# Kernel optimization log

Measured on AMD Instinct MI355X. Metric: run time of the kernel, lower is better.

The kernel has to match this reference:

```python
import jax, jax.numpy as jnp
import numpy as np

C = 512
GROUPS = 8
EPS = 1e-5


def setup_inputs() -> dict:
    key = jax.random.key(0)
    ks = jax.random.split(key, 11)
    B, H, W = 8, 64, 64
    x = jax.random.normal(ks[0], (B, C, H, W), dtype=jnp.float32)
    s = 1.0 / np.sqrt(C)
    return {
        "x": x,
        "gn_w": jnp.ones((C,), jnp.float32),
        "gn_b": jnp.zeros((C,), jnp.float32),
        "wq": jax.random.normal(ks[1], (C, C), jnp.float32) * s,
        "bq": jnp.zeros((C,), jnp.float32),
        "wk": jax.random.normal(ks[2], (C, C), jnp.float32) * s,
        "bk": jnp.zeros((C,), jnp.float32),
        "wv": jax.random.normal(ks[3], (C, C), jnp.float32) * s,
        "bv": jnp.zeros((C,), jnp.float32),
        "wo": jax.random.normal(ks[4], (C, C), jnp.float32) * s,
        "bo": jnp.zeros((C,), jnp.float32),
    }


def _group_norm(x, w, b):
    # x: [B, C, H, W], 8 groups over channel dim
    B, Ch, H, W = x.shape
    xg = x.reshape(B, GROUPS, Ch // GROUPS, H, W)
    mu = jnp.mean(xg, axis=(2, 3, 4), keepdims=True)
    var = jnp.var(xg, axis=(2, 3, 4), keepdims=True)
    xn = ((xg - mu) * jax.lax.rsqrt(var + EPS)).reshape(B, Ch, H, W)
    return xn * w[None, :, None, None] + b[None, :, None, None]


def reference(x, gn_w, gn_b, wq, bq, wk, bk, wv, bv, wo, bo):
    B, Ch, H, W = x.shape
    h = _group_norm(x, gn_w, gn_b)
    # [B, N, C] tokens, N = H*W
    h = h.reshape(B, Ch, H * W).transpose(0, 2, 1)
    q = jnp.einsum('bnc,dc->bnd', h, wq) + bq
    k = jnp.einsum('bnc,dc->bnd', h, wk) + bk
    v = jnp.einsum('bnc,dc->bnd', h, wv) + bv
    scores = jnp.einsum('bnd,bmd->bnm', q, k) / jnp.sqrt(jnp.float32(Ch))
    attn = jax.nn.softmax(scores, axis=-1)
    out = jnp.einsum('bnm,bmd->bnd', attn, v)
    out = jnp.einsum('bnd,ed->bne', out, wo) + bo
    out = out.transpose(0, 2, 1).reshape(B, Ch, H, W)
    return x + out
```

## Files before the change

### kernel.cpp

```cpp
#include <hip/hip_runtime.h>
#include <hip/hip_bf16.h>
#include <stdint.h>

typedef __hip_bfloat16 bf16;
typedef unsigned short u16;
typedef unsigned int u32;
using short8  = __attribute__((ext_vector_type(8))) short;
using short4v = __attribute__((ext_vector_type(4))) short;
using floatx4 = __attribute__((ext_vector_type(4))) float;
using uintx4  = __attribute__((ext_vector_type(4))) u32;

#define SCALE_L2E 0.06375872f

__device__ __forceinline__ float b2f(u16 u) {
  union { u32 i; float f; } v; v.i = ((u32)u) << 16; return v.f;
}
__device__ __forceinline__ u16 f2b(float f) {
  union { float f; u32 i; } v; v.f = f;
  u32 r = v.i + 0x7fffu + ((v.i >> 16) & 1u);
  return (u16)(r >> 16);
}

__device__ __forceinline__ void gl2lds16(const void* g, void* l) {
  __builtin_amdgcn_global_load_lds(
      (const __attribute__((address_space(1))) void*)g,
      (__attribute__((address_space(3))) void*)l,
      16, 0, 0);
}

__global__ __launch_bounds__(256)
void cvt_weights(const float* __restrict__ w0, const float* __restrict__ w1,
                 const float* __restrict__ w2, const float* __restrict__ w3,
                 u16* __restrict__ o0, u16* __restrict__ o1,
                 u16* __restrict__ o2, u16* __restrict__ o3)
{
  const float* w = blockIdx.y == 0 ? w0 : blockIdx.y == 1 ? w1 : blockIdx.y == 2 ? w2 : w3;
  u16* o = blockIdx.y == 0 ? o0 : blockIdx.y == 1 ? o1 : blockIdx.y == 2 ? o2 : o3;
  const int i = (blockIdx.x * 256 + threadIdx.x) * 4;
  floatx4 v = *(const floatx4*)(w + i);
  short4v p;
#pragma unroll
  for (int j = 0; j < 4; j++) p[j] = (short)f2b(v[j]);
  *(short4v*)(o + i) = p;
}

__global__ __launch_bounds__(256)
void gn_stats(const float* __restrict__ x, float* __restrict__ gmean, float* __restrict__ grstd)
{
  const int g = blockIdx.x, b = blockIdx.y;
  const float* base = x + ((long)(b * 512 + g * 64)) * 4096;
  const int t = threadIdx.x;
  float s = 0.f, ss = 0.f;
  for (int i = 0; i < 256; i++) {
    floatx4 v = *(const floatx4*)(base + i * 1024 + t * 4);
#pragma unroll
    for (int j = 0; j < 4; j++) { s += v[j]; ss += v[j] * v[j]; }
  }
  for (int off = 1; off < 64; off <<= 1) {
    s  += __shfl_xor(s, off, 64);
    ss += __shfl_xor(ss, off, 64);
  }
  __shared__ float as_[4], ass_[4];
  if ((t & 63) == 0) { as_[t >> 6] = s; ass_[t >> 6] = ss; }
  __syncthreads();
  if (t == 0) {
    float S1 = as_[0] + as_[1] + as_[2] + as_[3];
    float S2 = ass_[0] + ass_[1] + ass_[2] + ass_[3];
    const float inv = 1.0f / 262144.0f;
    float mu = S1 * inv;
    float var = S2 * inv - mu * mu;
    gmean[b * 8 + g] = mu;
    grstd[b * 8 + g] = rsqrtf(var + 1e-5f);
  }
}

__global__ __launch_bounds__(256)
void gn_apply(const float* __restrict__ x, const float* __restrict__ gw, const float* __restrict__ gb,
              const float* __restrict__ gmean, const float* __restrict__ grstd,
              bf16* __restrict__ h)
{
  const int b = blockIdx.z;
  const int c0 = blockIdx.y * 64;
  const int p0 = blockIdx.x * 64;
  const int t = threadIdx.x;
  const int c = c0 + (t & 63);
  const int g = c >> 6;
  const float mu = gmean[b * 8 + g], rs = grstd[b * 8 + g];
  const float wv = gw[c];
  const float bv = gb[c];
  const float a = rs * wv;
  const float bb = bv - mu * rs * wv;
  const float* xp = x + ((long)(b * 512 + c)) * 4096;
  u16* hp = (u16*)h + ((long)b * 4096) * 512 + c;
  const int pbase = p0 + (t >> 6);
#pragma unroll
  for (int i = 0; i < 16; i++) {
    int p = pbase + i * 4;
    float xv = xp[p];
    hp[(long)p * 512] = f2b(xv * a + bb);
  }
}

__global__ __launch_bounds__(256)
void pv_reduce(const bf16* __restrict__ part, const float* __restrict__ rl,
               bf16* __restrict__ o, long sOz, int RS)
{
  const int z = blockIdx.x;
  const long base = (long)blockIdx.y * 1024 + threadIdx.x * 4;
  const long slab = (long)RS * 512;
  const u16* p = (const u16*)part + (long)z * 4 * slab + base;
  floatx4 s = (floatx4)0.f;
#pragma unroll
  for (int sp = 0; sp < 4; sp++) {
    short4v v = *(const short4v*)(p + sp * slab);
#pragma unroll
    for (int j = 0; j < 4; j++) s[j] += b2f((u16)v[j]);
  }
  const float r = 1.0f / rl[z * RS + (int)(base >> 9)];
  short4v ov;
#pragma unroll
  for (int j = 0; j < 4; j++) ov[j] = (short)f2b(s[j] * r);
  *(short4v*)((u16*)o + (long)z * sOz + base) = ov;
}

constexpr int BM = 128, BN = 128, BK = 32;

template<int MODE>
__global__ __launch_bounds__(256)
void gemm_bt(const bf16* __restrict__ Ag, long sA,
             const bf16* __restrict__ Bg, long sB,
             const float* __restrict__ bias,
             const float* __restrict__ bias2,
             const float* __restrict__ bias3,
             const float* __restrict__ resid, long sR,
             bf16* __restrict__ Og, long sO, long sO2,
             float* __restrict__ rl,
             int M, int N, int K)
{
  __shared__ u16 As[2][BM * BK];
  __shared__ u16 Bs[2][BN * BK];
  const int t = threadIdx.x;
  const int bz = blockIdx.x;
  const int bm = blockIdx.y;
  int bn = blockIdx.z, sp = 0, kbeg = 0, kend = K;
  if (MODE == 3) { sp = bn >> 2; bn &= 3; kbeg = sp * 1024; kend = kbeg + 1024; }

  const u16* A = (const u16*)Ag + (long)bz * sA;
  const u16* B = (const u16*)Bg + (long)bz * sB;

  const int lane = t & 63, w = t >> 6;

  const int rs_ = w * 16 + (lane >> 2);
  const int seg = ((lane & 3) ^ ((rs_ >> 1) & 3)) * 8;
  const long aOff  = (long)(bm * BM + rs_) * K + seg;
  const long bOff  = (long)(bn * BN + rs_) * K + seg;
  const long aOff2 = aOff + 64L * K;
  const long bOff2 = bOff + 64L * K;
  const int wofs = w * 1024;

  const int wm = (w >> 1) * 64, wn = (w & 1) * 64;
  const int lc = lane & 15, quad = lane >> 4;

  int aoffs[4], boffs[4];
#pragma unroll
  for (int i = 0; i < 4; i++) {
    const int Ra = wm + i * 16 + lc;
    const int Rb = wn + i * 16 + lc;
    aoffs[i] = Ra * 64 + ((quad ^ ((Ra >> 1) & 3)) * 16);
    boffs[i] = Rb * 64 + ((quad ^ ((Rb >> 1) & 3)) * 16);
  }

  floatx4 acc[4][4];
#pragma unroll
  for (int i = 0; i < 4; i++)
#pragma unroll
    for (int j = 0; j < 4; j++) acc[i][j] = (floatx4)0.f;

  auto stage = [&](int buf, int kk) {
    char* aw = (char*)&As[buf][0] + wofs;
    char* bw = (char*)&Bs[buf][0] + wofs;
    gl2lds16(A + aOff  + kk, aw);
    gl2lds16(A + aOff2 + kk, aw + 4096);
    gl2lds16(B + bOff  + kk, bw);
    gl2lds16(B + bOff2 + kk, bw + 4096);
  };

  stage(0, kbeg);
  int cur = 0;
  for (int kk = kbeg; kk < kend; kk += BK) {
    __syncthreads();
    if (kk + BK < kend) stage(cur ^ 1, kk + BK);
    const char* Ac = (const char*)&As[cur][0];
    const char* Bc = (const char*)&Bs[cur][0];
    short8 af[4], bfr[4];
#pragma unroll
    for (int i = 0; i < 4; i++) af[i]  = *(const short8*)(Ac + aoffs[i]);
#pragma unroll
    for (int j = 0; j < 4; j++) bfr[j] = *(const short8*)(Bc + boffs[j]);
#pragma unroll
    for (int i = 0; i < 4; i++)
#pragma unroll
      for (int j = 0; j < 4; j++)
        acc[i][j] = __builtin_amdgcn_mfma_f32_16x16x32_bf16(af[i], bfr[j], acc[i][j], 0, 0, 0);
    cur ^= 1;
  }

#pragma unroll
  for (int i = 0; i < 4; i++) {
    const int gm0 = bm * BM + wm + i * 16 + quad * 4;
    if (MODE == 2) {
      u16* Ou = (u16*)(Og + (long)bz * sO);
      float rsum[4] = {0.f, 0.f, 0.f, 0.f};
#pragma unroll
      for (int j = 0; j < 4; j++) {
        const int gn = bn * BN + wn + j * 16 + lc;
        floatx4 a = acc[i][j];
#pragma unroll
        for (int rg = 0; rg < 4; rg++) {
          float p = exp2f(a[rg] * SCALE_L2E);
          rsum[rg] += p;
          Ou[(long)(gm0 + rg) * N + gn] = f2b(p);
        }
      }
#pragma unroll
      for (int rg = 0; rg < 4; rg++) {
        float s = rsum[rg];
        s += __shfl_xor(s, 1, 64);
        s += __shfl_xor(s, 2, 64);
        s += __shfl_xor(s, 4, 64);
        s += __shfl_xor(s, 8, 64);
        if (lc == 0) atomicAdd(&rl[(long)bz * M + gm0 + rg], s);
      }
    } else {
#pragma unroll
      for (int j = 0; j < 4; j++) {
        const int gn = bn * BN + wn + j * 16 + lc;
        floatx4 a = acc[i][j];
        if (MODE == 3) {
          u16* Ou = (u16*)Og + (long)(bz * 4 + sp) * sO;
#pragma unroll
          for (int rg = 0; rg < 4; rg++)
            Ou[(long)(gm0 + rg) * N + gn] = f2b(a[rg]);
        } else if (MODE == 4) {
          float* Of = (float*)Og + (long)bz * sO;
          const float bv = bias[gn];
          const float* Rz = resid + (long)bz * sR;
          const floatx4 rv = *(const floatx4*)&Rz[(long)gn * M + gm0];
          floatx4 p;
#pragma unroll
          for (int rg = 0; rg < 4; rg++) p[rg] = a[rg] + bv + rv[rg];
          *(floatx4*)&Of[(long)gn * M + gm0] = p;
        } else if (MODE == 5) {
          const int nt = gn >> 9;
          const int col = gn & 511;
          const float bvv = (nt == 0 ? bias : nt == 1 ? bias2 : bias3)[col];
          u16* Ou = (u16*)Og + (long)nt * sO2 + (long)bz * sO;
          if (nt < 2) {
#pragma unroll
            for (int rg = 0; rg < 4; rg++)
              Ou[(long)(gm0 + rg) * 512 + col] = f2b(a[rg] + bvv);
          } else {
            short4v p;
#pragma unroll
            for (int rg = 0; rg < 4; rg++) p[rg] = (short)f2b(a[rg] + bvv);
            *(short4v*)&Ou[(long)col * M + gm0] = p;
          }
        }
      }
    }
  }
}

extern "C" void kernel_launch(void* const* d_in, const int* in_sizes, int n_in,
                              void* d_out, int out_size, void* d_ws, size_t ws_size,
                              hipStream_t stream)
{
  const float* x  = (const float*)d_in[0];
  const float* gw = (const float*)d_in[1];
  const float* gb = (const float*)d_in[2];
  const float* wq = (const float*)d_in[3];
  const float* bq = (const float*)d_in[4];
  const float* wk = (const float*)d_in[5];
  const float* bk = (const float*)d_in[6];
  const float* wv = (const float*)d_in[7];
  const float* bv = (const float*)d_in[8];
  const float* wo = (const float*)d_in[9];
  const float* bo = (const float*)d_in[10];

  const long PB = (long)4096 * 512;

  auto need = [&](long nb, long rs) -> size_t {
    return (size_t)(4 * 262144 * 2
                  + nb * PB * 2 * 4
                  + nb * rs * 4096 * 2
                  + nb * 4 * rs * 512 * 2
                  + nb * 4096 * 4
                  + 8192);
  };
  const long cand_nB[4] = {8, 4, 2, 1};
  const long cand_RS[2] = {1024, 512};
  long nB = 1, RS = 512;
  bool found = false;
  for (int i = 0; i < 4 && !found; i++)
    for (int j = 0; j < 2 && !found; j++)
      if (need(cand_nB[i], cand_RS[j]) <= ws_size) { nB = cand_nB[i]; RS = cand_RS[j]; found = true; }

  char* ws = (char*)d_ws;
  u16*   wqb  = (u16*)ws;
  u16*   wkb  = wqb + 262144;
  u16*   wvb  = wkb + 262144;
  u16*   wob  = wvb + 262144;
  bf16*  h    = (bf16*)(wob + 262144);
  bf16*  q    = h  + nB * PB;
  bf16*  k    = q  + nB * PB;
  bf16*  vT   = k  + nB * PB;
  bf16*  o    = h;
  bf16*  S    = vT + nB * PB;
  bf16*  part = S + nB * RS * 4096;
  float* rl   = (float*)(part + nB * 4 * RS * 512);
  float* gm   = rl + nB * 4096;
  float* gr   = gm + 64;

  const long sS = RS * 4096;

  cvt_weights<<<dim3(256, 4), 256, 0, stream>>>(wq, wk, wv, wo, wqb, wkb, wvb, wob);
  gn_stats<<<dim3(8, 8), 256, 0, stream>>>(x, gm, gr);

  for (long b0 = 0; b0 < 8; b0 += nB) {
    const int gs = (int)nB;

    gn_apply<<<dim3(64, 8, gs), 256, 0, stream>>>(x + b0 * PB, gw, gb, gm + b0 * 8, gr + b0 * 8, h);
    hipMemsetAsync(rl, 0, (size_t)gs * 4096 * sizeof(float), stream);

    gemm_bt<5><<<dim3(gs, 32, 12), 256, 0, stream>>>(
        h, PB, (bf16*)wqb, 0, bq, bk, bv, nullptr, 0,
        q, PB, nB * PB, nullptr, 4096, 1536, 512);

    for (long r0 = 0; r0 < 4096; r0 += RS) {
      float* rli = rl + (r0 / RS) * (long)gs * RS;
      gemm_bt<2><<<dim3(gs, (int)(RS / 128), 32), 256, 0, stream>>>(
          q + r0 * 512, PB, k, PB, nullptr, nullptr, nullptr, nullptr, 0,
          S, sS, 0, rli, (int)RS, 4096, 512);
      gemm_bt<3><<<dim3(gs, (int)(RS / 128), 16), 256, 0, stream>>>(
          S, sS, vT, PB, nullptr, nullptr, nullptr, nullptr, 0,
          part, (long)RS * 512, 0, nullptr, (int)RS, 512, 4096);
      pv_reduce<<<dim3(gs, (int)(RS / 2)), 256, 0, stream>>>(
          part, rli, o + r0 * 512, PB, (int)RS);
    }

    gemm_bt<4><<<dim3(gs, 32, 4), 256, 0, stream>>>(
        o, PB, (bf16*)wob, 0, bo, nullptr, nullptr,
        x + b0 * PB, PB, (bf16*)((float*)d_out + b0 * PB), PB, 0, nullptr, 4096, 512, 512);
  }
}
```

Measured before the change: 792.7 us.

## Fuse QK, softmax and PV into one flash-style attention kernel

Replaces the separate score GEMM, split-K PV GEMM and reduction kernels with a single fused kernel. Each block computes a 128-query tile, streams 128-key chunks, exponentiates scores into LDS and accumulates the full 512-wide output in registers, normalizing by row sums at the end. This removes the global round trip of the score matrix, the partial buffers, the memset and the atomics. In exchange it has heavy register and LDS use, a grid of only one block per query tile, and reloads Q for every key chunk.

```diff
diff --git a/kernel.cpp b/kernel.cpp
--- a/kernel.cpp
+++ b/kernel.cpp
@@ -101,28 +101,6 @@
   }
 }
 
-__global__ __launch_bounds__(256)
-void pv_reduce(const bf16* __restrict__ part, const float* __restrict__ rl,
-               bf16* __restrict__ o, long sOz, int RS)
-{
-  const int z = blockIdx.x;
-  const long base = (long)blockIdx.y * 1024 + threadIdx.x * 4;
-  const long slab = (long)RS * 512;
-  const u16* p = (const u16*)part + (long)z * 4 * slab + base;
-  floatx4 s = (floatx4)0.f;
-#pragma unroll
-  for (int sp = 0; sp < 4; sp++) {
-    short4v v = *(const short4v*)(p + sp * slab);
-#pragma unroll
-    for (int j = 0; j < 4; j++) s[j] += b2f((u16)v[j]);
-  }
-  const float r = 1.0f / rl[z * RS + (int)(base >> 9)];
-  short4v ov;
-#pragma unroll
-  for (int j = 0; j < 4; j++) ov[j] = (short)f2b(s[j] * r);
-  *(short4v*)((u16*)o + (long)z * sOz + base) = ov;
-}
-
 constexpr int BM = 128, BN = 128, BK = 32;
 
 template<int MODE>
@@ -134,7 +112,6 @@
              const float* __restrict__ bias3,
              const float* __restrict__ resid, long sR,
              bf16* __restrict__ Og, long sO, long sO2,
-             float* __restrict__ rl,
              int M, int N, int K)
 {
   __shared__ u16 As[2][BM * BK];
@@ -142,8 +119,7 @@
   const int t = threadIdx.x;
   const int bz = blockIdx.x;
   const int bm = blockIdx.y;
-  int bn = blockIdx.z, sp = 0, kbeg = 0, kend = K;
-  if (MODE == 3) { sp = bn >> 2; bn &= 3; kbeg = sp * 1024; kend = kbeg + 1024; }
+  const int bn = blockIdx.z;
 
   const u16* A = (const u16*)Ag + (long)bz * sA;
   const u16* B = (const u16*)Bg + (long)bz * sB;
@@ -185,11 +161,11 @@
     gl2lds16(B + bOff2 + kk, bw + 4096);
   };
 
-  stage(0, kbeg);
+  stage(0, 0);
   int cur = 0;
-  for (int kk = kbeg; kk < kend; kk += BK) {
+  for (int kk = 0; kk < K; kk += BK) {
     __syncthreads();
-    if (kk + BK < kend) stage(cur ^ 1, kk + BK);
+    if (kk + BK < K) stage(cur ^ 1, kk + BK);
     const char* Ac = (const char*)&As[cur][0];
     const char* Bc = (const char*)&Bs[cur][0];
     short8 af[4], bfr[4];
@@ -208,67 +184,216 @@
 #pragma unroll
   for (int i = 0; i < 4; i++) {
     const int gm0 = bm * BM + wm + i * 16 + quad * 4;
-    if (MODE == 2) {
-      u16* Ou = (u16*)(Og + (long)bz * sO);
-      float rsum[4] = {0.f, 0.f, 0.f, 0.f};
-#pragma unroll
-      for (int j = 0; j < 4; j++) {
-        const int gn = bn * BN + wn + j * 16 + lc;
-        floatx4 a = acc[i][j];
-#pragma unroll
-        for (int rg = 0; rg < 4; rg++) {
-          float p = exp2f(a[rg] * SCALE_L2E);
-          rsum[rg] += p;
-          Ou[(long)(gm0 + rg) * N + gn] = f2b(p);
-        }
-      }
-#pragma unroll
-      for (int rg = 0; rg < 4; rg++) {
-        float s = rsum[rg];
-        s += __shfl_xor(s, 1, 64);
-        s += __shfl_xor(s, 2, 64);
-        s += __shfl_xor(s, 4, 64);
-        s += __shfl_xor(s, 8, 64);
-        if (lc == 0) atomicAdd(&rl[(long)bz * M + gm0 + rg], s);
-      }
-    } else {
-#pragma unroll
-      for (int j = 0; j < 4; j++) {
-        const int gn = bn * BN + wn + j * 16 + lc;
-        floatx4 a = acc[i][j];
-        if (MODE == 3) {
-          u16* Ou = (u16*)Og + (long)(bz * 4 + sp) * sO;
+#pragma unroll
+    for (int j = 0; j < 4; j++) {
+      const int gn = bn * BN + wn + j * 16 + lc;
+      floatx4 a = acc[i][j];
+      if (MODE == 4) {
+        float* Of = (float*)Og + (long)bz * sO;
+        const float bv = bias[gn];
+        const float* Rz = resid + (long)bz * sR;
+        const floatx4 rv = *(const floatx4*)&Rz[(long)gn * M + gm0];
+        floatx4 p;
+#pragma unroll
+        for (int rg = 0; rg < 4; rg++) p[rg] = a[rg] + bv + rv[rg];
+        *(floatx4*)&Of[(long)gn * M + gm0] = p;
+      } else {
+        const int nt = gn >> 9;
+        const int col = gn & 511;
+        const float bvv = (nt == 0 ? bias : nt == 1 ? bias2 : bias3)[col];
+        u16* Ou = (u16*)Og + (long)nt * sO2 + (long)bz * sO;
+        if (nt < 2) {
 #pragma unroll
           for (int rg = 0; rg < 4; rg++)
-            Ou[(long)(gm0 + rg) * N + gn] = f2b(a[rg]);
-        } else if (MODE == 4) {
-          float* Of = (float*)Og + (long)bz * sO;
-          const float bv = bias[gn];
-          const float* Rz = resid + (long)bz * sR;
-          const floatx4 rv = *(const floatx4*)&Rz[(long)gn * M + gm0];
-          floatx4 p;
-#pragma unroll
-          for (int rg = 0; rg < 4; rg++) p[rg] = a[rg] + bv + rv[rg];
-          *(floatx4*)&Of[(long)gn * M + gm0] = p;
-        } else if (MODE == 5) {
-          const int nt = gn >> 9;
-          const int col = gn & 511;
-          const float bvv = (nt == 0 ? bias : nt == 1 ? bias2 : bias3)[col];
-          u16* Ou = (u16*)Og + (long)nt * sO2 + (long)bz * sO;
-          if (nt < 2) {
-#pragma unroll
-            for (int rg = 0; rg < 4; rg++)
-              Ou[(long)(gm0 + rg) * 512 + col] = f2b(a[rg] + bvv);
-          } else {
-            short4v p;
-#pragma unroll
-            for (int rg = 0; rg < 4; rg++) p[rg] = (short)f2b(a[rg] + bvv);
-            *(short4v*)&Ou[(long)col * M + gm0] = p;
-          }
+            Ou[(long)(gm0 + rg) * 512 + col] = f2b(a[rg] + bvv);
+        } else {
+          short4v p;
+#pragma unroll
+          for (int rg = 0; rg < 4; rg++) p[rg] = (short)f2b(a[rg] + bvv);
+          *(short4v*)&Ou[(long)col * M + gm0] = p;
         }
       }
     }
   }
+}
+
+#define COMPUTE_SLAB(S, BUF)                                                \
+  {                                                                         \
+    _Pragma("unroll")                                                       \
+    for (int ks = 0; ks < 4; ks++) {                                        \
+      short8 vf[2], pf[4];                                                  \
+      _Pragma("unroll")                                                     \
+      for (int mf = 0; mf < 2; mf++) {                                      \
+        const int r = wr * 32 + mf * 16 + lc;                               \
+        vf[mf] = *(const short8*)((const char*)&vt_s[BUF][0] +              \
+                   r * 256 + (((ks * 4 + quad) ^ (r & 7)) * 16));           \
+      }                                                                     \
+      _Pragma("unroll")                                                     \
+      for (int nf = 0; nf < 4; nf++) {                                      \
+        const int r = wc * 64 + nf * 16 + lc;                               \
+        pf[nf] = *(const short8*)((const char*)p_s +                        \
+                   r * 256 + (((ks * 4 + quad) ^ (r & 7)) * 16));           \
+      }                                                                     \
+      _Pragma("unroll")                                                     \
+      for (int mf = 0; mf < 2; mf++)                                        \
+        _Pragma("unroll")                                                   \
+        for (int nf = 0; nf < 4; nf++)                                      \
+          acc_o[S][mf][nf] = __builtin_amdgcn_mfma_f32_16x16x32_bf16(       \
+              vf[mf], pf[nf], acc_o[S][mf][nf], 0, 0, 0);                   \
+    }                                                                       \
+  }
+
+__global__ __launch_bounds__(512, 2)
+void fused_attn(const bf16* __restrict__ qg, const bf16* __restrict__ kg,
+                const bf16* __restrict__ vtg, bf16* __restrict__ og)
+{
+  __shared__ u16 qk_s[2][2][128 * 32];
+  __shared__ u16 vt_s[2][128 * 128];
+  __shared__ u16 p_s[128 * 128];
+  __shared__ float rsum_s[4][128];
+
+  const int t = threadIdx.x;
+  const int lane = t & 63, w = t >> 6;
+  const int lc = lane & 15, quad = lane >> 4;
+  const int wr = w >> 1, wc = w & 1;
+  const int z = blockIdx.x, qt = blockIdx.y;
+  const long zoff = (long)z * (4096L * 512);
+  const u16* q_z  = (const u16*)qg + zoff;
+  const u16* k_z  = (const u16*)kg + zoff;
+  const u16* vt_z = (const u16*)vtg + zoff;
+  u16* o_z = (u16*)og + zoff;
+
+  const int srow = t >> 2;
+  const int sseg = ((t & 3) ^ ((srow >> 1) & 3)) * 8;
+  const u16* qsrc  = q_z + (long)(qt * 128 + srow) * 512 + sseg;
+  const u16* ksrcC = k_z + (long)srow * 512 + sseg;
+  const int vrow = t >> 4;
+  const int vseg = ((t & 15) ^ (vrow & 7)) * 8;
+  const u16* vsrcC = vt_z + (long)vrow * 4096 + vseg;
+
+  const int ldsbase = w * 1024;
+
+  int koff[2], qoff[4];
+#pragma unroll
+  for (int mf = 0; mf < 2; mf++) {
+    const int r = wr * 32 + mf * 16 + lc;
+    koff[mf] = r * 64 + ((quad ^ ((r >> 1) & 3)) * 16);
+  }
+#pragma unroll
+  for (int nf = 0; nf < 4; nf++) {
+    const int r = wc * 64 + nf * 16 + lc;
+    qoff[nf] = r * 64 + ((quad ^ ((r >> 1) & 3)) * 16);
+  }
+
+  auto stage_qk = [&](int buf, int ds) {
+    char* base = (char*)&qk_s[buf][0][0] + ldsbase;
+    gl2lds16(qsrc  + ds * 32, base);
+    gl2lds16(ksrcC + ds * 32, base + 8192);
+  };
+  auto stage_vt = [&](int buf, int slab) {
+    char* base = (char*)&vt_s[buf][0] + ldsbase;
+    const u16* vs = vsrcC + (long)slab * (128L * 4096);
+#pragma unroll
+    for (int i = 0; i < 4; i++)
+      gl2lds16(vs + (long)i * (32L * 4096), base + i * 8192);
+  };
+
+  floatx4 acc_o[4][2][4];
+#pragma unroll
+  for (int s = 0; s < 4; s++)
+#pragma unroll
+    for (int mf = 0; mf < 2; mf++)
+#pragma unroll
+      for (int nf = 0; nf < 4; nf++) acc_o[s][mf][nf] = (floatx4)0.f;
+  float rsum[4] = {0.f, 0.f, 0.f, 0.f};
+
+  for (int ck = 0; ck < 32; ++ck) {
+    floatx4 acc_s[2][4];
+#pragma unroll
+    for (int mf = 0; mf < 2; mf++)
+#pragma unroll
+      for (int nf = 0; nf < 4; nf++) acc_s[mf][nf] = (floatx4)0.f;
+
+    stage_qk(0, 0);
+#pragma unroll 2
+    for (int ds = 0; ds < 16; ++ds) {
+      __syncthreads();
+      if (ds < 15) stage_qk((ds + 1) & 1, ds + 1);
+      else         stage_vt(0, 0);
+      const int b = ds & 1;
+      const char* Kc = (const char*)&qk_s[b][1][0];
+      const char* Qc = (const char*)&qk_s[b][0][0];
+      short8 kf[2], qf[4];
+#pragma unroll
+      for (int mf = 0; mf < 2; mf++) kf[mf] = *(const short8*)(Kc + koff[mf]);
+#pragma unroll
+      for (int nf = 0; nf < 4; nf++) qf[nf] = *(const short8*)(Qc + qoff[nf]);
+#pragma unroll
+      for (int mf = 0; mf < 2; mf++)
+#pragma unroll
+        for (int nf = 0; nf < 4; nf++)
+          acc_s[mf][nf] = __builtin_amdgcn_mfma_f32_16x16x32_bf16(kf[mf], qf[nf], acc_s[mf][nf], 0, 0, 0);
+    }
+
+#pragma unroll
+    for (int mf = 0; mf < 2; mf++)
+#pragma unroll
+      for (int nf = 0; nf < 4; nf++) {
+        floatx4 a = acc_s[mf][nf];
+        float p0 = exp2f(a[0] * SCALE_L2E);
+        float p1 = exp2f(a[1] * SCALE_L2E);
+        float p2 = exp2f(a[2] * SCALE_L2E);
+        float p3 = exp2f(a[3] * SCALE_L2E);
+        rsum[nf] += (p0 + p1) + (p2 + p3);
+        short4v pk;
+        pk[0] = (short)f2b(p0); pk[1] = (short)f2b(p1);
+        pk[2] = (short)f2b(p2); pk[3] = (short)f2b(p3);
+        const int key0 = wr * 32 + mf * 16 + quad * 4;
+        const int qq = wc * 64 + nf * 16 + lc;
+        *(short4v*)((char*)p_s + qq * 256 + ((key0 * 2) ^ ((qq & 7) << 4))) = pk;
+      }
+
+    __syncthreads();
+    stage_vt(1, 1);
+    COMPUTE_SLAB(0, 0)
+    __syncthreads();
+    stage_vt(0, 2);
+    COMPUTE_SLAB(1, 1)
+    __syncthreads();
+    stage_vt(1, 3);
+    COMPUTE_SLAB(2, 0)
+    __syncthreads();
+    COMPUTE_SLAB(3, 1)
+
+    ksrcC += 128 * 512;
+    vsrcC += 128;
+  }
+
+#pragma unroll
+  for (int nf = 0; nf < 4; nf++) {
+    float s = rsum[nf];
+    s += __shfl_xor(s, 16, 64);
+    s += __shfl_xor(s, 32, 64);
+    if (lane < 16) rsum_s[wr][wc * 64 + nf * 16 + lane] = s;
+  }
+  __syncthreads();
+
+#pragma unroll
+  for (int s = 0; s < 4; s++)
+#pragma unroll
+    for (int mf = 0; mf < 2; mf++)
+#pragma unroll
+      for (int nf = 0; nf < 4; nf++) {
+        const int qq = wc * 64 + nf * 16 + lc;
+        const float tot = (rsum_s[0][qq] + rsum_s[1][qq]) + (rsum_s[2][qq] + rsum_s[3][qq]);
+        const float r = 1.0f / tot;
+        floatx4 a = acc_o[s][mf][nf];
+        short4v ov;
+#pragma unroll
+        for (int rg = 0; rg < 4; rg++) ov[rg] = (short)f2b(a[rg] * r);
+        const int d0 = s * 128 + wr * 32 + mf * 16 + quad * 4;
+        *(short4v*)&o_z[(long)(qt * 128 + qq) * 512 + d0] = ov;
+      }
 }
 
 extern "C" void kernel_launch(void* const* d_in, const int* in_sizes, int n_in,
@@ -289,21 +414,13 @@
 
   const long PB = (long)4096 * 512;
 
-  auto need = [&](long nb, long rs) -> size_t {
-    return (size_t)(4 * 262144 * 2
-                  + nb * PB * 2 * 4
-                  + nb * rs * 4096 * 2
-                  + nb * 4 * rs * 512 * 2
-                  + nb * 4096 * 4
-                  + 8192);
+  auto need = [&](long nb) -> size_t {
+    return (size_t)(4 * 262144 * 2 + nb * PB * 2 * 4 + 8192);
   };
+  long nB = 1;
   const long cand_nB[4] = {8, 4, 2, 1};
-  const long cand_RS[2] = {1024, 512};
-  long nB = 1, RS = 512;
-  bool found = false;
-  for (int i = 0; i < 4 && !found; i++)
-    for (int j = 0; j < 2 && !found; j++)
-      if (need(cand_nB[i], cand_RS[j]) <= ws_size) { nB = cand_nB[i]; RS = cand_RS[j]; found = true; }
+  for (int i = 0; i < 4; i++)
+    if (need(cand_nB[i]) <= ws_size) { nB = cand_nB[i]; break; }
 
   char* ws = (char*)d_ws;
   u16*   wqb  = (u16*)ws;
@@ -315,13 +432,8 @@
   bf16*  k    = q  + nB * PB;
   bf16*  vT   = k  + nB * PB;
   bf16*  o    = h;
-  bf16*  S    = vT + nB * PB;
-  bf16*  part = S + nB * RS * 4096;
-  float* rl   = (float*)(part + nB * 4 * RS * 512);
-  float* gm   = rl + nB * 4096;
+  float* gm   = (float*)(vT + nB * PB);
   float* gr   = gm + 64;
-
-  const long sS = RS * 4096;
 
   cvt_weights<<<dim3(256, 4), 256, 0, stream>>>(wq, wk, wv, wo, wqb, wkb, wvb, wob);
   gn_stats<<<dim3(8, 8), 256, 0, stream>>>(x, gm, gr);
@@ -330,26 +442,15 @@
     const int gs = (int)nB;
 
     gn_apply<<<dim3(64, 8, gs), 256, 0, stream>>>(x + b0 * PB, gw, gb, gm + b0 * 8, gr + b0 * 8, h);
-    hipMemsetAsync(rl, 0, (size_t)gs * 4096 * sizeof(float), stream);
 
     gemm_bt<5><<<dim3(gs, 32, 12), 256, 0, stream>>>(
         h, PB, (bf16*)wqb, 0, bq, bk, bv, nullptr, 0,
-        q, PB, nB * PB, nullptr, 4096, 1536, 512);
-
-    for (long r0 = 0; r0 < 4096; r0 += RS) {
-      float* rli = rl + (r0 / RS) * (long)gs * RS;
-      gemm_bt<2><<<dim3(gs, (int)(RS / 128), 32), 256, 0, stream>>>(
-          q + r0 * 512, PB, k, PB, nullptr, nullptr, nullptr, nullptr, 0,
-          S, sS, 0, rli, (int)RS, 4096, 512);
-      gemm_bt<3><<<dim3(gs, (int)(RS / 128), 16), 256, 0, stream>>>(
-          S, sS, vT, PB, nullptr, nullptr, nullptr, nullptr, 0,
-          part, (long)RS * 512, 0, nullptr, (int)RS, 512, 4096);
-      pv_reduce<<<dim3(gs, (int)(RS / 2)), 256, 0, stream>>>(
-          part, rli, o + r0 * 512, PB, (int)RS);
-    }
+        q, PB, nB * PB, 4096, 1536, 512);
+
+    fused_attn<<<dim3(gs, 32), 512, 0, stream>>>(q, k, vT, o);
 
     gemm_bt<4><<<dim3(gs, 32, 4), 256, 0, stream>>>(
         o, PB, (bf16*)wob, 0, bo, nullptr, nullptr,
-        x + b0 * PB, PB, (bf16*)((float*)d_out + b0 * PB), PB, 0, nullptr, 4096, 512, 512);
-  }
-}
+        x + b0 * PB, PB, (bf16*)((float*)d_out + b0 * PB), PB, 0, 4096, 512, 512);
+  }
+}
```

Measured after the change: 767.9 us. -3.1%, faster.
